# Kernel tuning notes

Hardware: AMD Instinct MI355X
Metric: run time of the kernel (lower is better)

The kernel has to match this reference:

```python
import jax, jax.numpy as jnp
import numpy as np

BETA = 1.0

def setup_inputs() -> dict:
    key = jax.random.key(0)
    k1, k2 = jax.random.split(key)
    N, E_DIM, N_E = 32768, 512, 8192
    z = jax.random.normal(k1, (N, E_DIM, 1, 1), dtype=jnp.float32)
    # nn.Embedding weight initialized uniform(-1, 1)
    embedding_weight = jax.random.uniform(k2, (N_E, E_DIM), dtype=jnp.float32, minval=-1.0, maxval=1.0)
    return {"z": z, "embedding_weight": embedding_weight}


def reference(z, embedding_weight):
    zf = z[:, :, 0, 0]                                  # [N, E]
    # squared euclidean distances [N, n_e]
    d = (jnp.sum(zf ** 2, axis=1, keepdims=True)
         + jnp.sum(embedding_weight ** 2, axis=1)
         - 2.0 * jnp.matmul(zf, embedding_weight.T))
    min_encoding_indices = jnp.argmin(d, axis=1)        # [N]
    z_q = embedding_weight[min_encoding_indices]        # [N, E]
    loss = (jnp.mean((jax.lax.stop_gradient(z_q) - zf) ** 2)
            + BETA * jnp.mean((z_q - jax.lax.stop_gradient(zf)) ** 2))
    # straight-through estimator
    z_q_st = zf + jax.lax.stop_gradient(z_q - zf)
    z_q_out = z_q_st[:, :, None, None]                  # [N, E, 1, 1]
    return loss, z_q_out, min_encoding_indices
```

## Files before the change

kernel.cpp:

```cpp
#include <hip/hip_runtime.h>
#include <hip/hip_fp16.h>
#include <float.h>

#define M_ROWS 32768
#define E_DIM  512
#define N_E    8192

#define BM 32
#define BN 128
#define NQ 4
#define EQ (N_E / NQ)

typedef __attribute__((ext_vector_type(8))) _Float16 half8;
typedef __attribute__((ext_vector_type(4))) float f32x4;

__device__ __forceinline__ void gl_lds16(const void* g, void* l) {
    __builtin_amdgcn_global_load_lds(
        (const __attribute__((address_space(1))) unsigned int*)g,
        (__attribute__((address_space(3))) unsigned int*)l, 16, 0, 0);
}

#define MFMA16(A_, B_, C_) __builtin_amdgcn_mfma_f32_16x16x32_f16((A_), (B_), (C_), 0, 0, 0)

__global__ __launch_bounds__(256) void f16_cast_kernel(const float* __restrict__ X,
                                                       ushort* __restrict__ H,
                                                       int n4) {
    int i = blockIdx.x * 256 + threadIdx.x;
    if (i >= n4) return;
    float4 v = ((const float4*)X)[i];
    float c[4] = {v.x, v.y, v.z, v.w};
    ushort hh[4];
    #pragma unroll
    for (int j = 0; j < 4; j++) {
        __half hb = __float2half(c[j]);
        hh[j] = *(ushort*)&hb;
    }
    ushort4 h = {hh[0], hh[1], hh[2], hh[3]};
    ((ushort4*)H)[i] = h;
}

__global__ __launch_bounds__(256) void pack_w_kernel(const float* __restrict__ W,
                                                     unsigned int* __restrict__ Wt) {
    __shared__ float Ws[16 * E_DIM];
    const int et = blockIdx.x;
    const int t = threadIdx.x;
    const float4* src = (const float4*)(W + (size_t)et * 16 * E_DIM);
    #pragma unroll
    for (int i = 0; i < 8; i++)
        ((float4*)Ws)[i * 256 + t] = src[i * 256 + t];
    __syncthreads();
    const int lane = t >> 2;
    const int col = lane & 15;
    const int koff = (lane >> 4) * 8 + (t & 3) * 2;
    unsigned int* dst = Wt + (size_t)et * 16 * 256 + t;
    #pragma unroll
    for (int kt = 0; kt < 16; kt++) {
        float f0 = Ws[col * E_DIM + kt * 32 + koff];
        float f1 = Ws[col * E_DIM + kt * 32 + koff + 1];
        __half h0 = __float2half(f0), h1 = __float2half(f1);
        unsigned int u = (unsigned int)(*(ushort*)&h0) | ((unsigned int)(*(ushort*)&h1) << 16);
        dst[kt * 256] = u;
    }
}

__global__ __launch_bounds__(256) void wnorm_kernel(const float* __restrict__ W,
                                                    float* __restrict__ wnorm) {
    int wave_id = (int)((blockIdx.x * blockDim.x + threadIdx.x) >> 6);
    int lane = threadIdx.x & 63;
    if (wave_id >= N_E) return;
    const float* row = W + (size_t)wave_id * E_DIM;
    float4 v0 = *(const float4*)(row + lane * 4);
    float4 v1 = *(const float4*)(row + 256 + lane * 4);
    float s = v0.x*v0.x + v0.y*v0.y + v0.z*v0.z + v0.w*v0.w
            + v1.x*v1.x + v1.y*v1.y + v1.z*v1.z + v1.w*v1.w;
    #pragma unroll
    for (int off = 32; off; off >>= 1) s += __shfl_down(s, off);
    if (lane == 0) wnorm[wave_id] = s;
}

struct Top2 { float v0, v1; int i0, i1; };

__device__ inline Top2 merge2(Top2 A, Top2 B) {
    bool af = (A.v0 < B.v0) || (A.v0 == B.v0 && A.i0 < B.i0);
    float Wv1 = af ? A.v1 : B.v1; int Wi1 = af ? A.i1 : B.i1;
    float Lv0 = af ? B.v0 : A.v0; int Li0 = af ? B.i0 : A.i0;
    bool s2 = (Wv1 < Lv0) || (Wv1 == Lv0 && Wi1 < Li0);
    Top2 R;
    R.v0 = af ? A.v0 : B.v0; R.i0 = af ? A.i0 : B.i0;
    R.v1 = s2 ? Wv1 : Lv0;   R.i1 = s2 ? Wi1 : Li0;
    return R;
}

__global__ __launch_bounds__(512, 2) void argmin_mfma(
        const ushort* __restrict__ Zh, const char* __restrict__ Wt,
        const float* __restrict__ wnorm, int* __restrict__ cand) {
    __shared__ __align__(16) char Lds[32768];

    const int t = threadIdx.x;
    const int lane = t & 63;
    const int wid = t >> 6;
    const int l15 = lane & 15, l4 = lane >> 4;

    const int id = blockIdx.x;
    const int orig = (id & 7) * 512 + (id >> 3);
    const int quarter = orig >> 10;
    const int rowblk = orig & 1023;
    const int row0 = rowblk * BM;
    const int ebase = quarter * EQ;

    const int arow = (t >> 2) & 31;
    const int aswz = (t & 3) ^ ((arow >> 1) & 3);
    const ushort* Ag = Zh + (size_t)(row0 + arow) * E_DIM + ((t >> 7) & 3) * 32 + aswz * 8;
    #pragma unroll
    for (int j = 0; j < 4; j++)
        gl_lds16(Ag + j * 128, Lds + j * 8192 + t * 16);

    asm volatile("s_waitcnt vmcnt(0)" ::: "memory");
    __builtin_amdgcn_s_barrier();
    __builtin_amdgcn_sched_barrier(0);

    const int kchunk_b = (l4 ^ ((l15 >> 1) & 3)) * 16;
    half8 Areg[32];
    #pragma unroll
    for (int ks = 0; ks < 16; ks++)
        #pragma unroll
        for (int mi = 0; mi < 2; mi++)
            Areg[ks * 2 + mi] = *(const half8*)(Lds + ks * 2048 + (mi * 16 + l15) * 64 + kchunk_b);
    asm volatile("s_waitcnt lgkmcnt(0)" ::: "memory");
    __builtin_amdgcn_sched_barrier(0);

    const char* Bp = Wt + ((size_t)(ebase >> 4) + wid) * 16384 + lane * 16;
    const float* wn_ptr = wnorm + ebase + wid * 16 + l15;

    float v0[8], v1[8];
    int i0[8], i1[8];
    #pragma unroll
    for (int q = 0; q < 8; q++) { v0[q] = FLT_MAX; v1[q] = FLT_MAX; i0[q] = 0; i1[q] = 0; }

    f32x4 acc[2];
    acc[0] = (f32x4){0.f, 0.f, 0.f, 0.f};
    acc[1] = (f32x4){0.f, 0.f, 0.f, 0.f};

    half8 Bbuf[8][2];

    #pragma unroll
    for (int p = 0; p < 7; p++) {
        Bbuf[p][0] = *(const half8*)(Bp + p * 2048);
        Bbuf[p][1] = *(const half8*)(Bp + p * 2048 + 1024);
    }

    for (int e0 = 0; e0 < 16; ++e0) {
        float wn = wn_ptr[0];

        #pragma unroll
        for (int Q = 0; Q < 8; Q++) {
            __builtin_amdgcn_s_setprio(1);
            acc[0] = MFMA16(Areg[4 * Q + 0], Bbuf[Q & 7][0], acc[0]);
            acc[1] = MFMA16(Areg[4 * Q + 1], Bbuf[Q & 7][0], acc[1]);
            acc[0] = MFMA16(Areg[4 * Q + 2], Bbuf[Q & 7][1], acc[0]);
            acc[1] = MFMA16(Areg[4 * Q + 3], Bbuf[Q & 7][1], acc[1]);
            __builtin_amdgcn_s_setprio(0);
            if (e0 < 15 || Q < 1) {
                const char* src = Bp + ((Q + 7) >> 3) * 131072 + ((Q + 7) & 7) * 2048;
                Bbuf[(Q + 7) & 7][0] = *(const half8*)(src);
                Bbuf[(Q + 7) & 7][1] = *(const half8*)(src + 1024);
            }
        }

        {
            int col = ebase + e0 * BN + wid * 16 + l15;
            #pragma unroll
            for (int mi = 0; mi < 2; mi++)
                #pragma unroll
                for (int r = 0; r < 4; r++) {
                    float sc = fmaf(-2.0f, acc[mi][r], wn);
                    int q = mi * 4 + r;
                    if (sc < v0[q])      { v1[q] = v0[q]; i1[q] = i0[q]; v0[q] = sc; i0[q] = col; }
                    else if (sc < v1[q]) { v1[q] = sc; i1[q] = col; }
                }
            acc[0] = (f32x4){0.f, 0.f, 0.f, 0.f};
            acc[1] = (f32x4){0.f, 0.f, 0.f, 0.f};
        }

        wn_ptr += BN;
        Bp += 131072;
    }

    __syncthreads();
    float4* SmTop = (float4*)Lds;

    #pragma unroll
    for (int mi = 0; mi < 2; mi++)
        #pragma unroll
        for (int r = 0; r < 4; r++) {
            int q = mi * 4 + r;
            Top2 T = {v0[q], v1[q], i0[q], i1[q]};
            #pragma unroll
            for (int mk = 1; mk <= 8; mk <<= 1) {
                Top2 O;
                O.v0 = __shfl_xor(T.v0, mk); O.v1 = __shfl_xor(T.v1, mk);
                O.i0 = __shfl_xor(T.i0, mk); O.i1 = __shfl_xor(T.i1, mk);
                T = merge2(T, O);
            }
            if (l15 == 0) {
                int rl = mi * 16 + l4 * 4 + r;
                SmTop[rl * 8 + wid] = make_float4(T.v0, __int_as_float(T.i0), T.v1, __int_as_float(T.i1));
            }
        }
    __syncthreads();
    if (t < BM) {
        Top2 q[8];
        #pragma unroll
        for (int j = 0; j < 8; j++) {
            float4 F = SmTop[t * 8 + j];
            q[j].v0 = F.x; q[j].i0 = __float_as_int(F.y);
            q[j].v1 = F.z; q[j].i1 = __float_as_int(F.w);
        }
        Top2 T = merge2(merge2(merge2(q[0], q[1]), merge2(q[2], q[3])),
                        merge2(merge2(q[4], q[5]), merge2(q[6], q[7])));
        cand[(size_t)(row0 + t) * (2 * NQ) + quarter * 2 + 0] = T.i0;
        cand[(size_t)(row0 + t) * (2 * NQ) + quarter * 2 + 1] = T.i1;
    }
}

__global__ __launch_bounds__(256) void rescore_gather_loss(
        const float* __restrict__ Z, const float* __restrict__ W,
        const float* __restrict__ wnorm, const int* __restrict__ cand,
        float* __restrict__ out, float* __restrict__ partials) {
    const int n = blockIdx.x;
    const int t = threadIdx.x;
    const int lane = t & 63, wv = t >> 6;
    int c[8];
    #pragma unroll
    for (int j = 0; j < 8; j++) c[j] = cand[(size_t)n * 8 + j];
    float2 zv = ((const float2*)(Z + (size_t)n * E_DIM))[t];
    float2 wvv[8];
    #pragma unroll
    for (int j = 0; j < 8; j++)
        wvv[j] = ((const float2*)(W + (size_t)c[j] * E_DIM))[t];
    __shared__ float red[4][8];
    #pragma unroll
    for (int j = 0; j < 8; j++) {
        float s = zv.x * wvv[j].x + zv.y * wvv[j].y;
        #pragma unroll
        for (int off = 32; off; off >>= 1) s += __shfl_down(s, off);
        if (lane == 0) red[wv][j] = s;
    }
    __syncthreads();
    float best = FLT_MAX; int bj = 0, bc = 0x7fffffff;
    #pragma unroll
    for (int j = 0; j < 8; j++) {
        float d = red[0][j] + red[1][j] + red[2][j] + red[3][j];
        float s = wnorm[c[j]] - 2.0f * d;
        if (s < best || (s == best && c[j] < bc)) { best = s; bj = j; bc = c[j]; }
    }
    float2 wq = wvv[0];
    #pragma unroll
    for (int j = 1; j < 8; j++) if (bj == j) wq = wvv[j];
    ((float2*)(out + 1 + (size_t)n * E_DIM))[t] = wq;
    float d0 = wq.x - zv.x, d1 = wq.y - zv.y;
    float sl = d0 * d0 + d1 * d1;
    #pragma unroll
    for (int off = 32; off; off >>= 1) sl += __shfl_down(sl, off);
    __shared__ float red2[4];
    if (lane == 0) red2[wv] = sl;
    __syncthreads();
    if (t == 0) {
        partials[n] = red2[0] + red2[1] + red2[2] + red2[3];
        out[1 + (size_t)M_ROWS * E_DIM + n] = (float)bc;
    }
}

__global__ __launch_bounds__(256) void loss_reduce_kernel(const float* __restrict__ partials,
                                                          float* __restrict__ out) {
    const int t = threadIdx.x;
    float s = 0.0f;
    for (int i = t; i < M_ROWS; i += 256) s += partials[i];
    #pragma unroll
    for (int off = 32; off; off >>= 1) s += __shfl_down(s, off);
    __shared__ float red[4];
    if ((t & 63) == 0) red[t >> 6] = s;
    __syncthreads();
    if (t == 0) {
        float total = red[0] + red[1] + red[2] + red[3];
        out[0] = 2.0f * total / ((float)M_ROWS * (float)E_DIM);
    }
}

extern "C" void kernel_launch(void* const* d_in, const int* in_sizes, int n_in,
                              void* d_out, int out_size, void* d_ws, size_t ws_size,
                              hipStream_t stream) {
    const float* Z = (const float*)d_in[0];
    const float* W = (const float*)d_in[1];
    float* out = (float*)d_out;

    char* p = (char*)d_ws;
    ushort* Zh = (ushort*)p;           p += (size_t)M_ROWS * E_DIM * 2;
    unsigned int* Wt = (unsigned int*)p; p += (size_t)N_E * E_DIM * 2;
    float* wnorm = (float*)p;          p += (size_t)N_E * 4;
    int* cand = (int*)p;               p += (size_t)M_ROWS * 8 * 4;
    float* partials = (float*)p;       p += (size_t)M_ROWS * 4;

    f16_cast_kernel<<<(M_ROWS * E_DIM / 4 + 255) / 256, 256, 0, stream>>>(Z, Zh, M_ROWS * E_DIM / 4);
    pack_w_kernel<<<N_E / 16, 256, 0, stream>>>(W, Wt);
    wnorm_kernel<<<N_E / 4, 256, 0, stream>>>(W, wnorm);
    argmin_mfma<<<NQ * (M_ROWS / BM), 512, 0, stream>>>(Zh, (const char*)Wt, wnorm, cand);
    rescore_gather_loss<<<M_ROWS, 256, 0, stream>>>(Z, W, wnorm, cand, out, partials);
    loss_reduce_kernel<<<1, 256, 0, stream>>>(partials, out);
}
```

Baseline: 595.2 us.

## Retile argmin kernel to 64-row blocks with 4 waves and more A reuse

The MFMA argmin kernel now gives each block 64 rows with 256 threads (4 waves) instead of 32 rows with 512 threads. Each wave holds 64 A fragments in registers and issues 4 MFMAs per B fragment, so every B load from the packed codebook is reused twice as often and total B traffic drops. The cost is much higher register pressure (64 half8 A regs plus 16 top-2 slots), a 64KB LDS staging buffer, and fewer blocks, which may hurt occupancy or cause spills.

```diff
diff --git a/kernel.cpp b/kernel.cpp
--- a/kernel.cpp
+++ b/kernel.cpp
@@ -6,8 +6,7 @@
 #define E_DIM  512
 #define N_E    8192
 
-#define BM 32
-#define BN 128
+#define BMR 64
 #define NQ 4
 #define EQ (N_E / NQ)
 
@@ -91,10 +90,10 @@
     return R;
 }
 
-__global__ __launch_bounds__(512, 2) void argmin_mfma(
+__global__ __launch_bounds__(256, 2) void argmin_mfma(
         const ushort* __restrict__ Zh, const char* __restrict__ Wt,
         const float* __restrict__ wnorm, int* __restrict__ cand) {
-    __shared__ __align__(16) char Lds[32768];
+    __shared__ __align__(16) char Lds[65536];
 
     const int t = threadIdx.x;
     const int lane = t & 63;
@@ -102,44 +101,44 @@
     const int l15 = lane & 15, l4 = lane >> 4;
 
     const int id = blockIdx.x;
-    const int orig = (id & 7) * 512 + (id >> 3);
-    const int quarter = orig >> 10;
-    const int rowblk = orig & 1023;
-    const int row0 = rowblk * BM;
+    const int orig = (id & 7) * 256 + (id >> 3);
+    const int quarter = orig >> 9;
+    const int rowblk = orig & 511;
+    const int row0 = rowblk * BMR;
     const int ebase = quarter * EQ;
 
-    const int arow = (t >> 2) & 31;
+    const int arow = (t >> 2) & 63;
     const int aswz = (t & 3) ^ ((arow >> 1) & 3);
-    const ushort* Ag = Zh + (size_t)(row0 + arow) * E_DIM + ((t >> 7) & 3) * 32 + aswz * 8;
-    #pragma unroll
-    for (int j = 0; j < 4; j++)
-        gl_lds16(Ag + j * 128, Lds + j * 8192 + t * 16);
+    const ushort* Ag = Zh + (size_t)(row0 + arow) * E_DIM + aswz * 8;
+    #pragma unroll
+    for (int j = 0; j < 16; j++)
+        gl_lds16(Ag + j * 32, Lds + j * 4096 + t * 16);
 
     asm volatile("s_waitcnt vmcnt(0)" ::: "memory");
     __builtin_amdgcn_s_barrier();
     __builtin_amdgcn_sched_barrier(0);
 
     const int kchunk_b = (l4 ^ ((l15 >> 1) & 3)) * 16;
-    half8 Areg[32];
+    half8 Areg[64];
     #pragma unroll
     for (int ks = 0; ks < 16; ks++)
         #pragma unroll
-        for (int mi = 0; mi < 2; mi++)
-            Areg[ks * 2 + mi] = *(const half8*)(Lds + ks * 2048 + (mi * 16 + l15) * 64 + kchunk_b);
+        for (int mi = 0; mi < 4; mi++)
+            Areg[ks * 4 + mi] = *(const half8*)(Lds + ks * 4096 + (mi * 16 + l15) * 64 + kchunk_b);
     asm volatile("s_waitcnt lgkmcnt(0)" ::: "memory");
     __builtin_amdgcn_sched_barrier(0);
 
     const char* Bp = Wt + ((size_t)(ebase >> 4) + wid) * 16384 + lane * 16;
     const float* wn_ptr = wnorm + ebase + wid * 16 + l15;
 
-    float v0[8], v1[8];
-    int i0[8], i1[8];
-    #pragma unroll
-    for (int q = 0; q < 8; q++) { v0[q] = FLT_MAX; v1[q] = FLT_MAX; i0[q] = 0; i1[q] = 0; }
-
-    f32x4 acc[2];
-    acc[0] = (f32x4){0.f, 0.f, 0.f, 0.f};
-    acc[1] = (f32x4){0.f, 0.f, 0.f, 0.f};
+    float v0[16], v1[16];
+    int i0[16], i1[16];
+    #pragma unroll
+    for (int q = 0; q < 16; q++) { v0[q] = FLT_MAX; v1[q] = FLT_MAX; i0[q] = 0; i1[q] = 0; }
+
+    f32x4 acc[4];
+    #pragma unroll
+    for (int mi = 0; mi < 4; mi++) acc[mi] = (f32x4){0.f, 0.f, 0.f, 0.f};
 
     half8 Bbuf[8][2];
 
@@ -149,28 +148,30 @@
         Bbuf[p][1] = *(const half8*)(Bp + p * 2048 + 1024);
     }
 
-    for (int e0 = 0; e0 < 16; ++e0) {
+    for (int s = 0; s < 32; ++s) {
         float wn = wn_ptr[0];
 
         #pragma unroll
         for (int Q = 0; Q < 8; Q++) {
             __builtin_amdgcn_s_setprio(1);
-            acc[0] = MFMA16(Areg[4 * Q + 0], Bbuf[Q & 7][0], acc[0]);
-            acc[1] = MFMA16(Areg[4 * Q + 1], Bbuf[Q & 7][0], acc[1]);
-            acc[0] = MFMA16(Areg[4 * Q + 2], Bbuf[Q & 7][1], acc[0]);
-            acc[1] = MFMA16(Areg[4 * Q + 3], Bbuf[Q & 7][1], acc[1]);
+            #pragma unroll
+            for (int mi = 0; mi < 4; mi++)
+                acc[mi] = MFMA16(Areg[8 * Q + mi], Bbuf[Q & 7][0], acc[mi]);
+            #pragma unroll
+            for (int mi = 0; mi < 4; mi++)
+                acc[mi] = MFMA16(Areg[8 * Q + 4 + mi], Bbuf[Q & 7][1], acc[mi]);
             __builtin_amdgcn_s_setprio(0);
-            if (e0 < 15 || Q < 1) {
-                const char* src = Bp + ((Q + 7) >> 3) * 131072 + ((Q + 7) & 7) * 2048;
+            if (s < 31 || Q < 1) {
+                const char* src = Bp + ((Q + 7) >> 3) * 65536 + ((Q + 7) & 7) * 2048;
                 Bbuf[(Q + 7) & 7][0] = *(const half8*)(src);
                 Bbuf[(Q + 7) & 7][1] = *(const half8*)(src + 1024);
             }
         }
 
         {
-            int col = ebase + e0 * BN + wid * 16 + l15;
-            #pragma unroll
-            for (int mi = 0; mi < 2; mi++)
+            int col = ebase + (s * 4 + wid) * 16 + l15;
+            #pragma unroll
+            for (int mi = 0; mi < 4; mi++)
                 #pragma unroll
                 for (int r = 0; r < 4; r++) {
                     float sc = fmaf(-2.0f, acc[mi][r], wn);
@@ -178,19 +179,19 @@
                     if (sc < v0[q])      { v1[q] = v0[q]; i1[q] = i0[q]; v0[q] = sc; i0[q] = col; }
                     else if (sc < v1[q]) { v1[q] = sc; i1[q] = col; }
                 }
-            acc[0] = (f32x4){0.f, 0.f, 0.f, 0.f};
-            acc[1] = (f32x4){0.f, 0.f, 0.f, 0.f};
+            #pragma unroll
+            for (int mi = 0; mi < 4; mi++) acc[mi] = (f32x4){0.f, 0.f, 0.f, 0.f};
         }
 
-        wn_ptr += BN;
-        Bp += 131072;
+        wn_ptr += 64;
+        Bp += 65536;
     }
 
     __syncthreads();
     float4* SmTop = (float4*)Lds;
 
     #pragma unroll
-    for (int mi = 0; mi < 2; mi++)
+    for (int mi = 0; mi < 4; mi++)
         #pragma unroll
         for (int r = 0; r < 4; r++) {
             int q = mi * 4 + r;
@@ -204,20 +205,19 @@
             }
             if (l15 == 0) {
                 int rl = mi * 16 + l4 * 4 + r;
-                SmTop[rl * 8 + wid] = make_float4(T.v0, __int_as_float(T.i0), T.v1, __int_as_float(T.i1));
+                SmTop[rl * 4 + wid] = make_float4(T.v0, __int_as_float(T.i0), T.v1, __int_as_float(T.i1));
             }
         }
     __syncthreads();
-    if (t < BM) {
-        Top2 q[8];
-        #pragma unroll
-        for (int j = 0; j < 8; j++) {
-            float4 F = SmTop[t * 8 + j];
+    if (t < BMR) {
+        Top2 q[4];
+        #pragma unroll
+        for (int j = 0; j < 4; j++) {
+            float4 F = SmTop[t * 4 + j];
             q[j].v0 = F.x; q[j].i0 = __float_as_int(F.y);
             q[j].v1 = F.z; q[j].i1 = __float_as_int(F.w);
         }
-        Top2 T = merge2(merge2(merge2(q[0], q[1]), merge2(q[2], q[3])),
-                        merge2(merge2(q[4], q[5]), merge2(q[6], q[7])));
+        Top2 T = merge2(merge2(q[0], q[1]), merge2(q[2], q[3]));
         cand[(size_t)(row0 + t) * (2 * NQ) + quarter * 2 + 0] = T.i0;
         cand[(size_t)(row0 + t) * (2 * NQ) + quarter * 2 + 1] = T.i1;
     }
@@ -295,16 +295,16 @@
     float* out = (float*)d_out;
 
     char* p = (char*)d_ws;
-    ushort* Zh = (ushort*)p;           p += (size_t)M_ROWS * E_DIM * 2;
+    ushort* Zh = (ushort*)p;             p += (size_t)M_ROWS * E_DIM * 2;
     unsigned int* Wt = (unsigned int*)p; p += (size_t)N_E * E_DIM * 2;
-    float* wnorm = (float*)p;          p += (size_t)N_E * 4;
-    int* cand = (int*)p;               p += (size_t)M_ROWS * 8 * 4;
-    float* partials = (float*)p;       p += (size_t)M_ROWS * 4;
+    float* wnorm = (float*)p;            p += (size_t)N_E * 4;
+    int* cand = (int*)p;                 p += (size_t)M_ROWS * 8 * 4;
+    float* partials = (float*)p;         p += (size_t)M_ROWS * 4;
 
     f16_cast_kernel<<<(M_ROWS * E_DIM / 4 + 255) / 256, 256, 0, stream>>>(Z, Zh, M_ROWS * E_DIM / 4);
     pack_w_kernel<<<N_E / 16, 256, 0, stream>>>(W, Wt);
     wnorm_kernel<<<N_E / 4, 256, 0, stream>>>(W, wnorm);
-    argmin_mfma<<<NQ * (M_ROWS / BM), 512, 0, stream>>>(Zh, (const char*)Wt, wnorm, cand);
+    argmin_mfma<<<NQ * (M_ROWS / BMR), 256, 0, stream>>>(Zh, (const char*)Wt, wnorm, cand);
     rescore_gather_loss<<<M_ROWS, 256, 0, stream>>>(Z, W, wnorm, cand, out, partials);
     loss_reduce_kernel<<<1, 256, 0, stream>>>(partials, out);
 }
```

Result: slower. 2.169 ms (+264.5%).
